# Performance work log

Measured on AMD Instinct MI355X. Metric: run time of the kernel, lower is better.

The kernel has to match this reference:

```python
import math
import jax, jax.numpy as jnp
import numpy as np

B_, L_, D_, N_, R_ = 4, 1024, 1024, 16, 64  # batch, seq, n_embd(=dim_inner), d_state, dt_rank


def setup_inputs() -> dict:
    key = jax.random.key(0)
    ks = jax.random.split(key, 6)
    s = lambda k, shp: jax.random.normal(k, shp, jnp.float32) * 0.02
    return {
        "x": jax.random.normal(ks[0], (B_, L_, D_), jnp.float32),
        "ln1_w": jnp.ones((D_,), jnp.float32),
        "ln2_w": jnp.ones((D_,), jnp.float32),
        "W_dbc": s(ks[1], (R_ + 2 * N_, D_)),   # x -> [delta_lowrank, B, C]
        "W_dt": s(ks[2], (D_, R_)),              # dt_rank -> dim_inner
        "b_dt": jnp.zeros((D_,), jnp.float32),
        "A_log": jnp.log(jnp.broadcast_to(jnp.arange(1, N_ + 1, dtype=jnp.float32), (D_, N_))),
        "Dp": jnp.ones((D_,), jnp.float32),      # skip-connection D parameter
        "W_fc": s(ks[3], (4 * D_, D_)),
        "W_proj": s(ks[4], (D_, 4 * D_)),
    }


def _layernorm(x, w):
    mu = jnp.mean(x, -1, keepdims=True)
    xc = x - mu
    var = jnp.mean(xc * xc, -1, keepdims=True)
    return xc * jax.lax.rsqrt(var + 1e-5) * w


def _new_gelu(x):
    c = math.sqrt(2.0 / math.pi)
    return 0.5 * x * (1.0 + jnp.tanh(c * (x + 0.044715 * x * x * x)))


def _ssm(x, W_dbc, W_dt, b_dt, A_log, Dp):
    # x: (b, l, d) with d == dim_inner == n_embd
    dbc = jnp.einsum("bld,ed->ble", x, W_dbc)                # (b,l,R+2N)
    delta, Bm, Cm = jnp.split(dbc, [R_, R_ + N_], axis=-1)
    delta = jax.nn.softplus(jnp.einsum("blr,dr->bld", delta, W_dt) + b_dt)  # (b,l,d)
    A = -jnp.exp(A_log)                                       # (d,n)
    dA = jnp.exp(delta[..., None] * A)                        # (b,l,d,n) discretized A
    dBx = (delta * x)[..., None] * Bm[:, :, None, :]          # (b,l,d,n) discretized B*x

    # h_t = dA_t * h_{t-1} + dBx_t  -> parallel first-order linear scan
    def combine(e1, e2):
        a1, b1 = e1
        a2, b2 = e2
        return a2 * a1, a2 * b1 + b2

    _, hs = jax.lax.associative_scan(combine, (dA, dBx), axis=1)
    y = jnp.einsum("bldn,bln->bld", hs, Cm)
    return y + x * Dp


def reference(x, ln1_w, ln2_w, W_dbc, W_dt, b_dt, A_log, Dp, W_fc, W_proj):
    h = jax.nn.softplus(_layernorm(x, ln1_w))
    h = h + _ssm(h, W_dbc, W_dt, b_dt, A_log, Dp)
    m = _layernorm(h, ln2_w)
    m = _new_gelu(jnp.einsum("bld,fd->blf", m, W_fc))
    m = jnp.einsum("blf,df->bld", m, W_proj)
    return h + m
```

## Files before the change

kernel.cpp:

```cpp
#include <hip/hip_runtime.h>
#include <cstdint>
#include <cstddef>

typedef unsigned short u16;
typedef unsigned int u32;
typedef __attribute__((ext_vector_type(8))) short short8;
typedef __attribute__((ext_vector_type(4))) float floatx4;
typedef __attribute__((ext_vector_type(4))) u16 u16x4;
typedef __attribute__((ext_vector_type(4))) u32 u32x4;

#define DEV static __device__ __forceinline__

DEV u16 f2b(float f){ u32 u = __float_as_uint(f); u32 r = u + 0x7fffu + ((u>>16)&1u); return (u16)(r>>16); }
DEV float softplusf(float z){ return fmaxf(z,0.f) + log1pf(__expf(-fabsf(z))); }
DEV float fast_tanhf(float u){ float e = __expf(2.f*u); return 1.f - 2.f/(e+1.f); }
DEV float geluf(float x){ float u = 0.7978845608028654f*(x + 0.044715f*x*x*x); return 0.5f*x*(1.f+fast_tanhf(u)); }

DEV void async_copy16(const void* gp, void* lp){
  __builtin_amdgcn_global_load_lds((const __attribute__((address_space(1))) u32*)gp,
                                   (__attribute__((address_space(3))) u32*)lp, 16, 0, 0);
}

DEV u32 ldsoff(const void* p){
  return (u32)(size_t)(const __attribute__((address_space(3))) char*)p;
}

DEV void ds_read128x4(u32 base, short8* dst){
  u32x4 r0, r1, r2, r3;
  asm volatile("ds_read_b128 %0, %4 offset:0\n\t"
               "ds_read_b128 %1, %4 offset:1024\n\t"
               "ds_read_b128 %2, %4 offset:2048\n\t"
               "ds_read_b128 %3, %4 offset:3072"
               : "=&v"(r0), "=&v"(r1), "=&v"(r2), "=&v"(r3)
               : "v"(base));
  union { u32x4 u; short8 s; } c0, c1, c2, c3;
  c0.u = r0; c1.u = r1; c2.u = r2; c3.u = r3;
  dst[0] = c0.s; dst[1] = c1.s; dst[2] = c2.s; dst[3] = c3.s;
}

__global__ __launch_bounds__(256)
void prep_weights(const float* __restrict__ Wdbc, const float* __restrict__ Wdt,
                  const float* __restrict__ Wfc, const float* __restrict__ Wproj,
                  u16* __restrict__ dbc_b, u16* __restrict__ dt_b,
                  u16* __restrict__ fc_b, u16* __restrict__ pj_b)
{
  int i = blockIdx.x*256 + threadIdx.x;
  const float* src; u16* dst; int j;
  if (i < 32768){
    int e = i*4, r = e >> 10;
    if (r >= 96){ u16x4 z = {0,0,0,0}; *(u16x4*)(dbc_b + e) = z; return; }
    src = Wdbc; dst = dbc_b; j = i;
  } else if (i < 49152){ src = Wdt;   dst = dt_b; j = i - 32768; }
  else if (i < 1097728){ src = Wfc;   dst = fc_b; j = i - 49152; }
  else                 { src = Wproj; dst = pj_b; j = i - 1097728; }
  float4 v = ((const float4*)src)[j];
  u16x4 o = { f2b(v.x), f2b(v.y), f2b(v.z), f2b(v.w) };
  *(u16x4*)(dst + j*4) = o;
}

__global__ void dbc_post(const float* __restrict__ p, u16* __restrict__ delta_in,
                         float* __restrict__ BCf){
  int e = blockIdx.x*256 + threadIdx.x;
  int t = e >> 7, c = e & 127;
  float s = 0.f;
  #pragma unroll
  for (int z=0;z<8;z++) s += p[(size_t)z*524288 + e];
  if (c < 64)      delta_in[t*64 + c] = f2b(s);
  else if (c < 96) BCf[t*32 + (c-64)] = s;
}

__global__ void proj_reduce(const float* __restrict__ p, const float* __restrict__ h1f,
                            float* __restrict__ out){
  int i = blockIdx.x*256 + threadIdx.x;
  float4 a = ((const float4*)p)[i];
  float4 b = ((const float4*)(p + (size_t) 4194304))[i];
  float4 c = ((const float4*)(p + (size_t) 8388608))[i];
  float4 d = ((const float4*)(p + (size_t)12582912))[i];
  float4 r = ((const float4*)h1f)[i];
  float4 o = make_float4(a.x+b.x+c.x+d.x+r.x, a.y+b.y+c.y+d.y+r.y,
                         a.z+b.z+c.z+d.z+r.z, a.w+b.w+c.w+d.w+r.w);
  ((float4*)out)[i] = o;
}

__global__ __launch_bounds__(256)
void ln1_kernel(const float* __restrict__ x, const float* __restrict__ w,
                float* __restrict__ h0f, u16* __restrict__ h0b)
{
  int row = blockIdx.x, tid = threadIdx.x;
  const float4* xr = (const float4*)(x + (size_t)row*1024);
  float4 v = xr[tid];
  float s1 = v.x+v.y+v.z+v.w;
  float s2 = v.x*v.x+v.y*v.y+v.z*v.z+v.w*v.w;
  #pragma unroll
  for (int m=1;m<64;m<<=1){ s1 += __shfl_xor(s1,m); s2 += __shfl_xor(s2,m); }
  __shared__ float red[8];
  int wv = tid>>6;
  if ((tid&63)==0){ red[wv]=s1; red[4+wv]=s2; }
  __syncthreads();
  s1 = red[0]+red[1]+red[2]+red[3];
  s2 = red[4]+red[5]+red[6]+red[7];
  float mu  = s1*(1.f/1024.f);
  float var = s2*(1.f/1024.f) - mu*mu;
  float rstd = rsqrtf(var + 1e-5f);
  float4 wv4 = ((const float4*)w)[tid];
  float o0 = softplusf((v.x-mu)*rstd*wv4.x);
  float o1 = softplusf((v.y-mu)*rstd*wv4.y);
  float o2 = softplusf((v.z-mu)*rstd*wv4.z);
  float o3 = softplusf((v.w-mu)*rstd*wv4.w);
  ((float4*)(h0f + (size_t)row*1024))[tid] = make_float4(o0,o1,o2,o3);
  u16x4 ob = { f2b(o0), f2b(o1), f2b(o2), f2b(o3) };
  *(u16x4*)(h0b + (size_t)row*1024 + tid*4) = ob;
}

__global__ __launch_bounds__(256)
void ln2_kernel(const float* __restrict__ x, const float* __restrict__ w,
                u16* __restrict__ outb)
{
  int row = blockIdx.x, tid = threadIdx.x;
  const float4* xr = (const float4*)(x + (size_t)row*1024);
  float4 v = xr[tid];
  float s1 = v.x+v.y+v.z+v.w;
  float s2 = v.x*v.x+v.y*v.y+v.z*v.z+v.w*v.w;
  #pragma unroll
  for (int m=1;m<64;m<<=1){ s1 += __shfl_xor(s1,m); s2 += __shfl_xor(s2,m); }
  __shared__ float red[8];
  int wv = tid>>6;
  if ((tid&63)==0){ red[wv]=s1; red[4+wv]=s2; }
  __syncthreads();
  s1 = red[0]+red[1]+red[2]+red[3];
  s2 = red[4]+red[5]+red[6]+red[7];
  float mu  = s1*(1.f/1024.f);
  float var = s2*(1.f/1024.f) - mu*mu;
  float rstd = rsqrtf(var + 1e-5f);
  float4 wv4 = ((const float4*)w)[tid];
  u16x4 ob = { f2b((v.x-mu)*rstd*wv4.x), f2b((v.y-mu)*rstd*wv4.y),
               f2b((v.z-mu)*rstd*wv4.z), f2b((v.w-mu)*rstd*wv4.w) };
  *(u16x4*)(outb + (size_t)row*1024 + tid*4) = ob;
}

template<int EPI, int SWZ>
__global__ __launch_bounds__(256)
void gemm_bt(const u16* __restrict__ A, int lda,
             const u16* __restrict__ B, int ldb, int K,
             float* __restrict__ outF, u16* __restrict__ outB, int ldo,
             const float* __restrict__ bias, size_t zstr)
{
  __shared__ u16 sA[128*32];
  __shared__ u16 sB[128*32];
  const int tid = threadIdx.x;
  int m_blk, n_blk, zb;
  if (SWZ == 0){ n_blk = blockIdx.x; m_blk = blockIdx.y; zb = blockIdx.z; }
  else if (SWZ == 1){
    int b = blockIdx.x, xcd = b & 7, local = b >> 3;
    m_blk = (xcd>>2)*16 + (local & 15);
    n_blk = (xcd&3)*8 + (local >> 4);
    zb = 0;
  } else {
    int b = blockIdx.x, xcd = b & 7, local = b >> 3;
    m_blk = (xcd>>1)*8 + (local & 7);
    n_blk = local >> 3;
    zb = xcd & 1;
  }
  const int m0 = m_blk*128, n0 = n_blk*128;
  const int kstart = zb * K;
  const int wave = tid>>6, lane = tid&63;
  const int wm = (wave>>1)*64, wn = (wave&1)*64;
  const int lr = lane&15, quad = lane>>4;

  floatx4 acc[4][4];
  #pragma unroll
  for (int i=0;i<4;i++)
    #pragma unroll
    for (int j=0;j<4;j++){ floatx4 z = {0.f,0.f,0.f,0.f}; acc[i][j]=z; }

  const int r0 = tid>>2;
  const int kc8 = (((tid&3) ^ ((tid>>3)&3)))*8;
  const int sswz = ((lr>>1)&3);
  for (int k0=kstart; k0<kstart+K; k0+=32){
    __syncthreads();
    async_copy16(A + (size_t)(m0+r0)*lda    + k0+kc8, &sA[(size_t)tid*8]);
    async_copy16(A + (size_t)(m0+64+r0)*lda + k0+kc8, &sA[(size_t)(tid+256)*8]);
    async_copy16(B + (size_t)(n0+r0)*ldb    + k0+kc8, &sB[(size_t)tid*8]);
    async_copy16(B + (size_t)(n0+64+r0)*ldb + k0+kc8, &sB[(size_t)(tid+256)*8]);
    __syncthreads();
    short8 af[4], bf[4];
    #pragma unroll
    for (int i=0;i<4;i++){
      af[i] = *(const short8*)&sA[(wm+i*16+lr)*32 + (quad^sswz)*8];
      bf[i] = *(const short8*)&sB[(wn+i*16+lr)*32 + (quad^sswz)*8];
    }
    #pragma unroll
    for (int i=0;i<4;i++)
      #pragma unroll
      for (int j=0;j<4;j++)
        acc[i][j] = __builtin_amdgcn_mfma_f32_16x16x32_bf16(af[i], bf[j], acc[i][j], 0,0,0);
  }
  #pragma unroll
  for (int i=0;i<4;i++){
    #pragma unroll
    for (int j=0;j<4;j++){
      #pragma unroll
      for (int r=0;r<4;r++){
        int gr = m0 + wm + i*16 + quad*4 + r;
        int gc = n0 + wn + j*16 + lr;
        float v = acc[i][j][r];
        size_t o = (size_t)gr*ldo + gc;
        if (EPI==1)      outF[o] = softplusf(v + bias[gc]);
        else if (EPI==2) outB[o] = f2b(geluf(v));
        else             outF[zstr*zb + o] = v;
      }
    }
  }
}

template<int EPI, int SWZ>
__global__ __launch_bounds__(512, 2)
void gemm256(const u16* __restrict__ A, int lda,
             const u16* __restrict__ B, int ldb, int K,
             float* __restrict__ outF, u16* __restrict__ outB, int ldo,
             size_t zstr)
{
  __shared__ u16 sA[2][4][4096];
  __shared__ u16 sB[2][4][4096];
  const int tid = threadIdx.x;
  int m_blk, n_blk, zb;
  if (SWZ == 3){
    int b = blockIdx.x, xcd = b & 7, local = b >> 3;
    m_blk = (xcd>>2)*8 + (local & 7);
    n_blk = (xcd&3)*4 + (local >> 3);
    zb = 0;
  } else {
    int b = blockIdx.x, xcd = b & 7, local = b >> 3;
    zb    = xcd >> 1;
    m_blk = (xcd&1)*8 + (local & 7);
    n_blk = local >> 3;
  }
  const int m0 = m_blk*256, n0 = n_blk*256;
  const int kstart = zb*K;
  const int wave = tid>>6, lane = tid&63;
  const int mq = wave>>2, nq = wave&3;
  const int lr = lane&15, quad = lane>>4;
  const int sswz = (lr>>1)&3;

  const int srow = tid>>2;
  const int scol = ((tid&3) ^ ((tid>>3)&3))*8;
  const u16* pa = A + (size_t)(m0 + srow)*lda + scol;
  const u16* pb = B + (size_t)(n0 + srow)*ldb + scol;
  u16* la = (u16*)sA + tid*8;
  u16* lb = (u16*)sB + tid*8;
  const size_t ah128 = (size_t)128*lda;
  const size_t bh128 = (size_t)128*ldb;

  const int a_rd = (mq*64 + lr)*32 + (quad^sswz)*8;
  const int b_rd = ((nq&1)*64 + lr)*32 + (quad^sswz)*8;
  const int bun  = nq>>1;
  const u32 a_rdB = ldsoff(sA) + (u32)(a_rd*2);
  const u32 b_rdB = ldsoff(sB) + (u32)(b_rd*2) + (u32)(bun*8192);

  floatx4 acc[2][4][4];
  #pragma unroll
  for (int h=0;h<2;h++)
    #pragma unroll
    for (int i=0;i<4;i++)
      #pragma unroll
      for (int j=0;j<4;j++){ floatx4 z={0.f,0.f,0.f,0.f}; acc[h][i][j]=z; }

  short8 af[2][4], bf[2][4];

#define STG_A(NB,KS,H,KT) async_copy16(pa + (size_t)(H)*ah128 + (size_t)((KT) + (KS)*32), \
                                       la + (NB)*16384 + ((KS)*2+(H))*4096)
#define STG_B(NB,KS,H,KT) async_copy16(pb + (size_t)(H)*bh128 + (size_t)((KT) + (KS)*32), \
                                       lb + (NB)*16384 + ((KS)*2+(H))*4096)

#define PH(MFS, MBS, AH, PRBUF, PRKS, PRAH, PRB, VM, LG, STMTS)               \
  {                                                                           \
    STMTS;                                                                    \
    asm volatile("s_waitcnt vmcnt(" VM ")" ::: "memory");                     \
    __builtin_amdgcn_s_barrier();                                             \
    ds_read128x4(a_rdB + (PRBUF)*32768u + (PRKS)*16384u + (PRAH)*8192u,       \
                 af[(MFS)^1]);                                                \
    if (PRB)                                                                  \
      ds_read128x4(b_rdB + (PRBUF)*32768u + (PRKS)*16384u, bf[(MBS)^1]);      \
    asm volatile("s_waitcnt lgkmcnt(" LG ")" ::: "memory");                   \
    __builtin_amdgcn_sched_barrier(0);                                        \
    __builtin_amdgcn_s_setprio(1);                                            \
    _Pragma("unroll")                                                         \
    for (int i_=0;i_<4;i_++)                                                  \
      _Pragma("unroll")                                                       \
      for (int j_=0;j_<4;j_++)                                                \
        acc[AH][i_][j_] = __builtin_amdgcn_mfma_f32_16x16x32_bf16(            \
            af[MFS][i_], bf[MBS][j_], acc[AH][i_][j_], 0,0,0);                \
    __builtin_amdgcn_s_setprio(0);                                            \
  }

  STG_A(0,0,0,kstart); STG_B(0,0,0,kstart);
  STG_B(0,0,1,kstart); STG_A(0,0,1,kstart);
  STG_B(0,1,0,kstart); STG_B(0,1,1,kstart);
  STG_A(0,1,0,kstart); STG_A(0,1,1,kstart);
  asm volatile("s_waitcnt vmcnt(5)" ::: "memory");
  __builtin_amdgcn_s_barrier();
  ds_read128x4(a_rdB, af[0]);
  ds_read128x4(b_rdB, bf[0]);

  const int NT = K >> 6;
  for (int t=0; t<NT; t+=2){
    const int ka = kstart + (t+1)*64;
    const int kb = (t+2 < NT) ? (kstart + (t+2)*64) : kstart;
    PH(0,0,0, 0,0,1,0, "6","4", STG_A(1,0,0,ka); STG_B(1,0,0,ka));
    PH(1,0,1, 0,1,0,1, "5","8", STG_B(1,0,1,ka); STG_A(1,0,1,ka));
    PH(0,1,0, 0,1,1,0, "6","4", STG_B(1,1,0,ka); STG_B(1,1,1,ka));
    PH(1,1,1, 1,0,0,1, "5","8", STG_A(1,1,0,ka); STG_A(1,1,1,ka));
    PH(0,0,0, 1,0,1,0, "6","4", STG_A(0,0,0,kb); STG_B(0,0,0,kb));
    PH(1,0,1, 1,1,0,1, "5","8", STG_B(0,0,1,kb); STG_A(0,0,1,kb));
    PH(0,1,0, 1,1,1,0, "6","4", STG_B(0,1,0,kb); STG_B(0,1,1,kb));
    PH(1,1,1, 0,0,0,1, "5","8", STG_A(0,1,0,kb); STG_A(0,1,1,kb));
  }

#undef PH
#undef STG_A
#undef STG_B

  #pragma unroll
  for (int h=0;h<2;h++){
    #pragma unroll
    for (int i=0;i<4;i++){
      #pragma unroll
      for (int j=0;j<4;j++){
        #pragma unroll
        for (int r=0;r<4;r++){
          int gr = m0 + h*128 + mq*64 + i*16 + quad*4 + r;
          int gc = n0 + nq*64 + j*16 + lr;
          float v = acc[h][i][j][r];
          size_t o = (size_t)gr*ldo + gc;
          if (EPI==2) outB[o] = f2b(geluf(v));
          else        outF[zstr*zb + o] = v;
        }
      }
    }
  }
}

__global__ __launch_bounds__(256)
void scan_p1(const float* __restrict__ delta, const float* __restrict__ h0f,
             const float* __restrict__ BCf, const float* __restrict__ A_log,
             float* __restrict__ Pbuf, float* __restrict__ Sbuf)
{
  int blk = blockIdx.x;
  int d = (blk & 3)*256 + threadIdx.x;
  int c = (blk >> 2) & 31;
  int b = blk >> 7;
  float a2[16], h[16], P[16];
  #pragma unroll
  for (int n=0;n<16;n++){ a2[n] = -__expf(A_log[d*16+n]) * 1.44269504f; h[n]=0.f; P[n]=1.f; }
  int t0 = c*32;
  const float* dptr = delta + ((size_t)(b*1024 + t0))*1024 + d;
  const float* xptr = h0f   + ((size_t)(b*1024 + t0))*1024 + d;
  const float* bc   = BCf   + ((size_t)(b*1024 + t0))*32;
  #pragma unroll 4
  for (int t=0;t<32;t++){
    float dlt = dptr[t*1024];
    float xv  = xptr[t*1024];
    float dx = dlt*xv;
    #pragma unroll
    for (int n=0;n<16;n++){
      float dA = exp2f(dlt*a2[n]);
      h[n] = dA*h[n] + dx*bc[t*32+n];
      P[n] *= dA;
    }
  }
  size_t base = ((size_t)((b*32 + c)*16))*1024 + d;
  #pragma unroll
  for (int n=0;n<16;n++){ Pbuf[base + (size_t)n*1024] = P[n]; Sbuf[base + (size_t)n*1024] = h[n]; }
}

__global__ __launch_bounds__(256)
void scan_p2(const float* __restrict__ Pbuf, const float* __restrict__ Sbuf,
             float* __restrict__ Hbuf)
{
  int blk = blockIdx.x;
  int d = (blk & 3)*256 + threadIdx.x;
  int n = (blk >> 2) & 15;
  int b = blk >> 6;
  float H = 0.f;
  for (int c=0;c<32;c++){
    size_t idx = ((size_t)((b*32 + c)*16 + n))*1024 + d;
    float P = Pbuf[idx], S = Sbuf[idx];
    Hbuf[idx] = H;
    H = P*H + S;
  }
}

__global__ __launch_bounds__(256)
void scan_p3(const float* __restrict__ delta, const float* __restrict__ h0f,
             const float* __restrict__ BCf, const float* __restrict__ A_log,
             const float* __restrict__ Hbuf, const float* __restrict__ Dp,
             float* __restrict__ h1f)
{
  int blk = blockIdx.x;
  int d = (blk & 3)*256 + threadIdx.x;
  int c = (blk >> 2) & 31;
  int b = blk >> 7;
  float a2[16], h[16];
  size_t hb = ((size_t)((b*32 + c)*16))*1024 + d;
  #pragma unroll
  for (int n=0;n<16;n++){
    a2[n] = -__expf(A_log[d*16+n]) * 1.44269504f;
    h[n] = Hbuf[hb + (size_t)n*1024];
  }
  float dpv = 1.f + Dp[d];
  int t0 = c*32;
  const float* dptr = delta + ((size_t)(b*1024 + t0))*1024 + d;
  const float* xptr = h0f   + ((size_t)(b*1024 + t0))*1024 + d;
  const float* bc   = BCf   + ((size_t)(b*1024 + t0))*32;
  float* optr = h1f + ((size_t)(b*1024 + t0))*1024 + d;
  #pragma unroll 4
  for (int t=0;t<32;t++){
    float dlt = dptr[t*1024];
    float xv  = xptr[t*1024];
    float dx = dlt*xv;
    float y = 0.f;
    #pragma unroll
    for (int n=0;n<16;n++){
      float dA = exp2f(dlt*a2[n]);
      h[n] = dA*h[n] + dx*bc[t*32+n];
      y += h[n]*bc[t*32+16+n];
    }
    optr[t*1024] = xv*dpv + y;
  }
}

extern "C" void kernel_launch(void* const* d_in, const int* in_sizes, int n_in,
                              void* d_out, int out_size, void* d_ws, size_t ws_size,
                              hipStream_t stream)
{
  const float* x    = (const float*)d_in[0];
  const float* ln1w = (const float*)d_in[1];
  const float* ln2w = (const float*)d_in[2];
  const float* Wdbc = (const float*)d_in[3];
  const float* Wdt  = (const float*)d_in[4];
  const float* bdt  = (const float*)d_in[5];
  const float* Alog = (const float*)d_in[6];
  const float* Dp   = (const float*)d_in[7];
  const float* Wfc  = (const float*)d_in[8];
  const float* Wproj= (const float*)d_in[9];
  float* out = (float*)d_out;

  char* ws = (char*)d_ws;
  size_t off = 0;
  auto carve = [&](size_t bytes)->char*{ char* p = ws + off; off += (bytes + 255) & ~(size_t)255; return p; };
  const size_t T = 4096;
  float* h0f   = (float*)carve(T*1024*4);
  float* h1f   = (float*)carve(T*1024*4);
  float* dlt   = (float*)carve(T*1024*4);
  float* Pbuf  = (float*)carve((size_t)4*32*16*1024*4);
  float* Sbuf  = (float*)carve((size_t)4*32*16*1024*4);
  float* Hbuf  = (float*)carve((size_t)4*32*16*1024*4);
  float* pad_  = (float*)carve((size_t)4*32*16*1024*4);
  float* BCf   = (float*)carve(T*32*4);
  u16*   h0b   = (u16*)  carve(T*1024*2);
  u16*   m0b   = (u16*)  carve(T*1024*2);
  u16*   g_b   = (u16*)  carve(T*4096*2);
  u16*   din_b = (u16*)  carve(T*64*2);
  u16*   Wdbc_b= (u16*)  carve((size_t)128*1024*2);
  u16*   Wdt_b = (u16*)  carve((size_t)1024*64*2);
  u16*   Wfc_b = (u16*)  carve((size_t)4096*1024*2);
  u16*   Wpj_b = (u16*)  carve((size_t)1024*4096*2);
  float* dbc_p  = Hbuf;
  float* proj_p = dlt;
  (void)pad_; (void)ws_size; (void)in_sizes; (void)n_in; (void)out_size;

  prep_weights<<<8384, 256, 0, stream>>>(Wdbc, Wdt, Wfc, Wproj,
                                         Wdbc_b, Wdt_b, Wfc_b, Wpj_b);

  ln1_kernel<<<4096, 256, 0, stream>>>(x, ln1w, h0f, h0b);

  gemm_bt<4,0><<<dim3(1,32,8), 256, 0, stream>>>(h0b, 1024, Wdbc_b, 1024, 128,
                                                 dbc_p, nullptr, 128, nullptr, (size_t)T*128);
  dbc_post<<<2048, 256, 0, stream>>>(dbc_p, din_b, BCf);

  gemm_bt<1,0><<<dim3(8,32), 256, 0, stream>>>(din_b, 64, Wdt_b, 64, 64,
                                               dlt, nullptr, 1024, bdt, 0);

  scan_p1<<<512, 256, 0, stream>>>(dlt, h0f, BCf, Alog, Pbuf, Sbuf);
  scan_p2<<<256, 256, 0, stream>>>(Pbuf, Sbuf, Hbuf);
  scan_p3<<<512, 256, 0, stream>>>(dlt, h0f, BCf, Alog, Hbuf, Dp, h1f);

  ln2_kernel<<<4096, 256, 0, stream>>>(h1f, ln2w, m0b);

  gemm256<2,3><<<256, 512, 0, stream>>>(m0b, 1024, Wfc_b, 1024, 1024,
                                        nullptr, g_b, 4096, 0);

  gemm256<4,4><<<256, 512, 0, stream>>>(g_b, 4096, Wpj_b, 4096, 1024,
                                        proj_p, nullptr, 1024, (size_t)T*1024);
  proj_reduce<<<4096, 256, 0, stream>>>(proj_p, h1f, out);
}
```

Measured before the change: 330.1 us.

## Fuse split-K projection reduction via atomics into output and halve scan chunk count

The projection GEMM's split-K partial results are no longer written to a scratch buffer and summed by a separate reduce kernel. Each split-K slice now atomically adds into the output, which scan_p3 pre-initialises with the residual h1. This removes one kernel launch and roughly 80 MB of partial-sum traffic, at the cost of float atomics and a summation order that is not deterministic. Separately, the scan chunk length goes from 32 to 64 steps, halving the number of blocks in p1 and p3 and the length of the p2 carry chain, which lowers parallelism in those kernels.

New measurement: 363.1 us. +10.0%, slower.

```diff
diff --git a/kernel.cpp b/kernel.cpp
--- a/kernel.cpp
+++ b/kernel.cpp
@@ -67,19 +67,6 @@
   for (int z=0;z<8;z++) s += p[(size_t)z*524288 + e];
   if (c < 64)      delta_in[t*64 + c] = f2b(s);
   else if (c < 96) BCf[t*32 + (c-64)] = s;
-}
-
-__global__ void proj_reduce(const float* __restrict__ p, const float* __restrict__ h1f,
-                            float* __restrict__ out){
-  int i = blockIdx.x*256 + threadIdx.x;
-  float4 a = ((const float4*)p)[i];
-  float4 b = ((const float4*)(p + (size_t) 4194304))[i];
-  float4 c = ((const float4*)(p + (size_t) 8388608))[i];
-  float4 d = ((const float4*)(p + (size_t)12582912))[i];
-  float4 r = ((const float4*)h1f)[i];
-  float4 o = make_float4(a.x+b.x+c.x+d.x+r.x, a.y+b.y+c.y+d.y+r.y,
-                         a.z+b.z+c.z+d.z+r.z, a.w+b.w+c.w+d.w+r.w);
-  ((float4*)out)[i] = o;
 }
 
 __global__ __launch_bounds__(256)
@@ -217,8 +204,7 @@
 __global__ __launch_bounds__(512, 2)
 void gemm256(const u16* __restrict__ A, int lda,
              const u16* __restrict__ B, int ldb, int K,
-             float* __restrict__ outF, u16* __restrict__ outB, int ldo,
-             size_t zstr)
+             float* __restrict__ outF, u16* __restrict__ outB, int ldo)
 {
   __shared__ u16 sA[2][4][4096];
   __shared__ u16 sB[2][4][4096];
@@ -333,7 +319,7 @@
           float v = acc[h][i][j][r];
           size_t o = (size_t)gr*ldo + gc;
           if (EPI==2) outB[o] = f2b(geluf(v));
-          else        outF[zstr*zb + o] = v;
+          else        unsafeAtomicAdd(outF + o, v);
         }
       }
     }
@@ -347,17 +333,17 @@
 {
   int blk = blockIdx.x;
   int d = (blk & 3)*256 + threadIdx.x;
-  int c = (blk >> 2) & 31;
-  int b = blk >> 7;
+  int c = (blk >> 2) & 15;
+  int b = blk >> 6;
   float a2[16], h[16], P[16];
   #pragma unroll
   for (int n=0;n<16;n++){ a2[n] = -__expf(A_log[d*16+n]) * 1.44269504f; h[n]=0.f; P[n]=1.f; }
-  int t0 = c*32;
+  int t0 = c*64;
   const float* dptr = delta + ((size_t)(b*1024 + t0))*1024 + d;
   const float* xptr = h0f   + ((size_t)(b*1024 + t0))*1024 + d;
   const float* bc   = BCf   + ((size_t)(b*1024 + t0))*32;
   #pragma unroll 4
-  for (int t=0;t<32;t++){
+  for (int t=0;t<64;t++){
     float dlt = dptr[t*1024];
     float xv  = xptr[t*1024];
     float dx = dlt*xv;
@@ -368,7 +354,7 @@
       P[n] *= dA;
     }
   }
-  size_t base = ((size_t)((b*32 + c)*16))*1024 + d;
+  size_t base = ((size_t)((b*16 + c)*16))*1024 + d;
   #pragma unroll
   for (int n=0;n<16;n++){ Pbuf[base + (size_t)n*1024] = P[n]; Sbuf[base + (size_t)n*1024] = h[n]; }
 }
@@ -382,8 +368,8 @@
   int n = (blk >> 2) & 15;
   int b = blk >> 6;
   float H = 0.f;
-  for (int c=0;c<32;c++){
-    size_t idx = ((size_t)((b*32 + c)*16 + n))*1024 + d;
+  for (int c=0;c<16;c++){
+    size_t idx = ((size_t)((b*16 + c)*16 + n))*1024 + d;
     float P = Pbuf[idx], S = Sbuf[idx];
     Hbuf[idx] = H;
     H = P*H + S;
@@ -394,27 +380,28 @@
 void scan_p3(const float* __restrict__ delta, const float* __restrict__ h0f,
              const float* __restrict__ BCf, const float* __restrict__ A_log,
              const float* __restrict__ Hbuf, const float* __restrict__ Dp,
-             float* __restrict__ h1f)
+             float* __restrict__ h1f, float* __restrict__ outp)
 {
   int blk = blockIdx.x;
   int d = (blk & 3)*256 + threadIdx.x;
-  int c = (blk >> 2) & 31;
-  int b = blk >> 7;
+  int c = (blk >> 2) & 15;
+  int b = blk >> 6;
   float a2[16], h[16];
-  size_t hb = ((size_t)((b*32 + c)*16))*1024 + d;
+  size_t hb = ((size_t)((b*16 + c)*16))*1024 + d;
   #pragma unroll
   for (int n=0;n<16;n++){
     a2[n] = -__expf(A_log[d*16+n]) * 1.44269504f;
     h[n] = Hbuf[hb + (size_t)n*1024];
   }
   float dpv = 1.f + Dp[d];
-  int t0 = c*32;
+  int t0 = c*64;
   const float* dptr = delta + ((size_t)(b*1024 + t0))*1024 + d;
   const float* xptr = h0f   + ((size_t)(b*1024 + t0))*1024 + d;
   const float* bc   = BCf   + ((size_t)(b*1024 + t0))*32;
-  float* optr = h1f + ((size_t)(b*1024 + t0))*1024 + d;
+  float* optr = h1f  + ((size_t)(b*1024 + t0))*1024 + d;
+  float* wptr = outp + ((size_t)(b*1024 + t0))*1024 + d;
   #pragma unroll 4
-  for (int t=0;t<32;t++){
+  for (int t=0;t<64;t++){
     float dlt = dptr[t*1024];
     float xv  = xptr[t*1024];
     float dx = dlt*xv;
@@ -425,7 +412,9 @@
       h[n] = dA*h[n] + dx*bc[t*32+n];
       y += h[n]*bc[t*32+16+n];
     }
-    optr[t*1024] = xv*dpv + y;
+    float hv = xv*dpv + y;
+    optr[t*1024] = hv;
+    wptr[t*1024] = hv;
   }
 }
 
@@ -466,7 +455,6 @@
   u16*   Wfc_b = (u16*)  carve((size_t)4096*1024*2);
   u16*   Wpj_b = (u16*)  carve((size_t)1024*4096*2);
   float* dbc_p  = Hbuf;
-  float* proj_p = dlt;
   (void)pad_; (void)ws_size; (void)in_sizes; (void)n_in; (void)out_size;
 
   prep_weights<<<8384, 256, 0, stream>>>(Wdbc, Wdt, Wfc, Wproj,
@@ -481,16 +469,15 @@
   gemm_bt<1,0><<<dim3(8,32), 256, 0, stream>>>(din_b, 64, Wdt_b, 64, 64,
                                                dlt, nullptr, 1024, bdt, 0);
 
-  scan_p1<<<512, 256, 0, stream>>>(dlt, h0f, BCf, Alog, Pbuf, Sbuf);
+  scan_p1<<<256, 256, 0, stream>>>(dlt, h0f, BCf, Alog, Pbuf, Sbuf);
   scan_p2<<<256, 256, 0, stream>>>(Pbuf, Sbuf, Hbuf);
-  scan_p3<<<512, 256, 0, stream>>>(dlt, h0f, BCf, Alog, Hbuf, Dp, h1f);
+  scan_p3<<<256, 256, 0, stream>>>(dlt, h0f, BCf, Alog, Hbuf, Dp, h1f, out);
 
   ln2_kernel<<<4096, 256, 0, stream>>>(h1f, ln2w, m0b);
 
   gemm256<2,3><<<256, 512, 0, stream>>>(m0b, 1024, Wfc_b, 1024, 1024,
-                                        nullptr, g_b, 4096, 0);
+                                        nullptr, g_b, 4096);
 
   gemm256<4,4><<<256, 512, 0, stream>>>(g_b, 4096, Wpj_b, 4096, 1024,
-                                        proj_p, nullptr, 1024, (size_t)T*1024);
-  proj_reduce<<<4096, 256, 0, stream>>>(proj_p, h1f, out);
-}
+                                        out, nullptr, 1024);
+}
```

## Fuse split-K projection reduce and residual add into atomic adds on output

Applied to the files above, without the earlier changes.

The scan writes the residual h1 straight into the output buffer, and the split-K projection GEMM adds its partial results into that buffer with float atomics. This removes the separate reduce kernel, the partial-sum workspace and the h1 buffer, so four partial tensors are no longer written and read back. The block mapping for split-K is also reordered so that the four K-splits of a tile sit on the same XCD. In exchange, every output element takes four unordered atomic adds, which makes the summation order nondeterministic and puts atomic traffic through L2.

Measured after the change: 359.7 us. 9.0% more time.

```diff
diff --git a/kernel.cpp b/kernel.cpp
--- a/kernel.cpp
+++ b/kernel.cpp
@@ -67,19 +67,6 @@
   for (int z=0;z<8;z++) s += p[(size_t)z*524288 + e];
   if (c < 64)      delta_in[t*64 + c] = f2b(s);
   else if (c < 96) BCf[t*32 + (c-64)] = s;
-}
-
-__global__ void proj_reduce(const float* __restrict__ p, const float* __restrict__ h1f,
-                            float* __restrict__ out){
-  int i = blockIdx.x*256 + threadIdx.x;
-  float4 a = ((const float4*)p)[i];
-  float4 b = ((const float4*)(p + (size_t) 4194304))[i];
-  float4 c = ((const float4*)(p + (size_t) 8388608))[i];
-  float4 d = ((const float4*)(p + (size_t)12582912))[i];
-  float4 r = ((const float4*)h1f)[i];
-  float4 o = make_float4(a.x+b.x+c.x+d.x+r.x, a.y+b.y+c.y+d.y+r.y,
-                         a.z+b.z+c.z+d.z+r.z, a.w+b.w+c.w+d.w+r.w);
-  ((float4*)out)[i] = o;
 }
 
 __global__ __launch_bounds__(256)
@@ -217,8 +204,7 @@
 __global__ __launch_bounds__(512, 2)
 void gemm256(const u16* __restrict__ A, int lda,
              const u16* __restrict__ B, int ldb, int K,
-             float* __restrict__ outF, u16* __restrict__ outB, int ldo,
-             size_t zstr)
+             float* __restrict__ outF, u16* __restrict__ outB, int ldo)
 {
   __shared__ u16 sA[2][4][4096];
   __shared__ u16 sB[2][4][4096];
@@ -231,9 +217,9 @@
     zb = 0;
   } else {
     int b = blockIdx.x, xcd = b & 7, local = b >> 3;
-    zb    = xcd >> 1;
+    n_blk = xcd >> 1;
     m_blk = (xcd&1)*8 + (local & 7);
-    n_blk = local >> 3;
+    zb    = local >> 3;
   }
   const int m0 = m_blk*256, n0 = n_blk*256;
   const int kstart = zb*K;
@@ -333,7 +319,7 @@
           float v = acc[h][i][j][r];
           size_t o = (size_t)gr*ldo + gc;
           if (EPI==2) outB[o] = f2b(geluf(v));
-          else        outF[zstr*zb + o] = v;
+          else        unsafeAtomicAdd(outF + o, v);
         }
       }
     }
@@ -394,7 +380,7 @@
 void scan_p3(const float* __restrict__ delta, const float* __restrict__ h0f,
              const float* __restrict__ BCf, const float* __restrict__ A_log,
              const float* __restrict__ Hbuf, const float* __restrict__ Dp,
-             float* __restrict__ h1f)
+             float* __restrict__ outp)
 {
   int blk = blockIdx.x;
   int d = (blk & 3)*256 + threadIdx.x;
@@ -412,7 +398,7 @@
   const float* dptr = delta + ((size_t)(b*1024 + t0))*1024 + d;
   const float* xptr = h0f   + ((size_t)(b*1024 + t0))*1024 + d;
   const float* bc   = BCf   + ((size_t)(b*1024 + t0))*32;
-  float* optr = h1f + ((size_t)(b*1024 + t0))*1024 + d;
+  float* wptr = outp + ((size_t)(b*1024 + t0))*1024 + d;
   #pragma unroll 4
   for (int t=0;t<32;t++){
     float dlt = dptr[t*1024];
@@ -425,7 +411,7 @@
       h[n] = dA*h[n] + dx*bc[t*32+n];
       y += h[n]*bc[t*32+16+n];
     }
-    optr[t*1024] = xv*dpv + y;
+    wptr[t*1024] = xv*dpv + y;
   }
 }
 
@@ -450,7 +436,6 @@
   auto carve = [&](size_t bytes)->char*{ char* p = ws + off; off += (bytes + 255) & ~(size_t)255; return p; };
   const size_t T = 4096;
   float* h0f   = (float*)carve(T*1024*4);
-  float* h1f   = (float*)carve(T*1024*4);
   float* dlt   = (float*)carve(T*1024*4);
   float* Pbuf  = (float*)carve((size_t)4*32*16*1024*4);
   float* Sbuf  = (float*)carve((size_t)4*32*16*1024*4);
@@ -466,7 +451,6 @@
   u16*   Wfc_b = (u16*)  carve((size_t)4096*1024*2);
   u16*   Wpj_b = (u16*)  carve((size_t)1024*4096*2);
   float* dbc_p  = Hbuf;
-  float* proj_p = dlt;
   (void)pad_; (void)ws_size; (void)in_sizes; (void)n_in; (void)out_size;
 
   prep_weights<<<8384, 256, 0, stream>>>(Wdbc, Wdt, Wfc, Wproj,
@@ -483,14 +467,13 @@
 
   scan_p1<<<512, 256, 0, stream>>>(dlt, h0f, BCf, Alog, Pbuf, Sbuf);
   scan_p2<<<256, 256, 0, stream>>>(Pbuf, Sbuf, Hbuf);
-  scan_p3<<<512, 256, 0, stream>>>(dlt, h0f, BCf, Alog, Hbuf, Dp, h1f);
-
-  ln2_kernel<<<4096, 256, 0, stream>>>(h1f, ln2w, m0b);
+  scan_p3<<<512, 256, 0, stream>>>(dlt, h0f, BCf, Alog, Hbuf, Dp, out);
+
+  ln2_kernel<<<4096, 256, 0, stream>>>(out, ln2w, m0b);
 
   gemm256<2,3><<<256, 512, 0, stream>>>(m0b, 1024, Wfc_b, 1024, 1024,
-                                        nullptr, g_b, 4096, 0);
+                                        nullptr, g_b, 4096);
 
   gemm256<4,4><<<256, 512, 0, stream>>>(g_b, 4096, Wpj_b, 4096, 1024,
-                                        proj_p, nullptr, 1024, (size_t)T*1024);
-  proj_reduce<<<4096, 256, 0, stream>>>(proj_p, h1f, out);
-}
+                                        out, nullptr, 1024);
+}
```
